# Kernel tuning notes

Measured on AMD Instinct MI355X. Metric: run time of the kernel, lower is better.

The kernel has to match this reference:

```python
import jax, jax.numpy as jnp
import numpy as np

NSIDE = 128
NPIX = 12 * NSIDE * NSIDE          # HEALPix pixel count, nested ordering
WIN = 16                           # window = 4x4 nested child block (w=1)
SHIFT = WIN // 2
EPS = 1e-5


def _ln(x, g, b):
    mu = x.mean(-1, keepdims=True)
    var = ((x - mu) ** 2).mean(-1, keepdims=True)
    return (x - mu) * jax.lax.rsqrt(var + EPS) * g + b


def _window_attn(x, wq, bq, wp, bp, n_heads):
    B, N, C = x.shape
    D = C // n_heads
    nw = N // WIN
    qkv = (x @ wq + bq).reshape(B, nw, WIN, 3, n_heads, D)
    q, k, v = jnp.moveaxis(qkv, 3, 0)
    q = jnp.swapaxes(q, 2, 3)
    k = jnp.swapaxes(k, 2, 3)
    v = jnp.swapaxes(v, 2, 3)
    scores = jnp.einsum('bwhqd,bwhkd->bwhqk', q, k) * (D ** -0.5)
    attn = jax.nn.softmax(scores, axis=-1)
    out = jnp.einsum('bwhqk,bwhkd->bwhqd', attn, v)
    out = jnp.swapaxes(out, 2, 3).reshape(B, N, C)
    return out @ wp + bp


def _transformer_block(x, p, shift, n_heads):
    if shift:
        x = jnp.roll(x, -SHIFT, axis=1)          # cyclic shift along nested index
    x = x + _window_attn(_ln(x, p['ln1_g'], p['ln1_b']),
                         p['w_qkv'], p['b_qkv'], p['w_proj'], p['b_proj'], n_heads)
    h = _ln(x, p['ln2_g'], p['ln2_b'])
    x = x + jax.nn.gelu(h @ p['w_mlp1'] + p['b_mlp1'], approximate=False) @ p['w_mlp2'] + p['b_mlp2']
    if shift:
        x = jnp.roll(x, SHIFT, axis=1)
    return x


def _forward(x, w_ff1, b_ff1, ln1_g, ln1_b, w_qkv, b_qkv, w_proj, b_proj,
             ln2_g, ln2_b, w_mlp1, b_mlp1, w_mlp2, b_mlp2, w_ff2, b_ff2,
             n_heads=4):
    residual = x
    h = jax.nn.gelu(x @ w_ff1 + b_ff1, approximate=False)
    for i, shift in enumerate((False, True)):
        p = dict(ln1_g=ln1_g[i], ln1_b=ln1_b[i], w_qkv=w_qkv[i], b_qkv=b_qkv[i],
                 w_proj=w_proj[i], b_proj=b_proj[i], ln2_g=ln2_g[i], ln2_b=ln2_b[i],
                 w_mlp1=w_mlp1[i], b_mlp1=b_mlp1[i], w_mlp2=w_mlp2[i], b_mlp2=b_mlp2[i])
        h = _transformer_block(h, p, shift, n_heads)
    return residual + h @ w_ff2 + b_ff2


def setup_inputs() -> dict:
    key = jax.random.key(0)
    ks = jax.random.split(key, 8)
    F, C, M = 64, 128, 512  # node_feat_dim, node_hidden_dim, mlp hidden
    s = 0.02
    return {
        'x': jax.random.normal(ks[0], (1, NPIX, F), jnp.float32),
        'w_ff1': jax.random.normal(ks[1], (F, C), jnp.float32) * s,
        'b_ff1': jnp.zeros((C,), jnp.float32),
        'ln1_g': jnp.ones((2, C), jnp.float32),
        'ln1_b': jnp.zeros((2, C), jnp.float32),
        'w_qkv': jax.random.normal(ks[2], (2, C, 3 * C), jnp.float32) * s,
        'b_qkv': jnp.zeros((2, 3 * C), jnp.float32),
        'w_proj': jax.random.normal(ks[3], (2, C, C), jnp.float32) * s,
        'b_proj': jnp.zeros((2, C), jnp.float32),
        'ln2_g': jnp.ones((2, C), jnp.float32),
        'ln2_b': jnp.zeros((2, C), jnp.float32),
        'w_mlp1': jax.random.normal(ks[4], (2, C, M), jnp.float32) * s,
        'b_mlp1': jnp.zeros((2, M), jnp.float32),
        'w_mlp2': jax.random.normal(ks[5], (2, M, C), jnp.float32) * s,
        'b_mlp2': jnp.zeros((2, C), jnp.float32),
        'w_ff2': jax.random.normal(ks[6], (C, F), jnp.float32) * s,
        'b_ff2': jnp.zeros((F,), jnp.float32),
    }


def reference(x, w_ff1, b_ff1, ln1_g, ln1_b, w_qkv, b_qkv, w_proj, b_proj,
              ln2_g, ln2_b, w_mlp1, b_mlp1, w_mlp2, b_mlp2, w_ff2, b_ff2):
    return _forward(x, w_ff1, b_ff1, ln1_g, ln1_b, w_qkv, b_qkv, w_proj, b_proj,
                    ln2_g, ln2_b, w_mlp1, b_mlp1, w_mlp2, b_mlp2, w_ff2, b_ff2)
```

## Files before the change

### kernel.cpp

```cpp
#include <hip/hip_runtime.h>
#include <hip/hip_bf16.h>
#include <math.h>

#define NPIX 196608
#define SCALE_Q 0.17677669529663687f

typedef __attribute__((ext_vector_type(4))) float f32x4;
typedef __attribute__((ext_vector_type(8))) short short8;
typedef __attribute__((ext_vector_type(4))) short short4v;
typedef __hip_bfloat16 bf16;

__device__ __forceinline__ float gelu_f(float x) {
    float yy = 1.5957691216057308f * (x + 0.044715f * x * x * x);
    float e = __expf(yy);
    return x - x * __builtin_amdgcn_rcpf(e + 1.0f);
}
__device__ __forceinline__ float gelu_fast(float x) {
    float e = __expf(-1.702f * x);
    return x * __builtin_amdgcn_rcpf(1.0f + e);
}

__device__ __forceinline__ short bfbits(float f) {
    bf16 h = __float2bfloat16(f);
    return *reinterpret_cast<short*>(&h);
}

__device__ __forceinline__ short8 ldsA(const bf16* buf, int row, int el) {
    return *reinterpret_cast<const short8*>(buf + row * 128 + (el ^ ((row & 7) << 3)));
}
__device__ __forceinline__ short8 ldsA64(const bf16* buf, int row, int el) {
    return *reinterpret_cast<const short8*>(buf + row * 64 + (el ^ ((row & 7) << 3)));
}
__device__ __forceinline__ short8 gld8(const bf16* p) {
    return *reinterpret_cast<const short8*>(p);
}

__device__ __forceinline__ void bar_lds() {
    asm volatile("s_waitcnt lgkmcnt(0)" ::: "memory");
    __builtin_amdgcn_s_barrier();
}

__global__ __launch_bounds__(256) void k_convert(
    const float* __restrict__ wff1, const float* __restrict__ wqkv,
    const float* __restrict__ wproj, const float* __restrict__ wmlp1,
    const float* __restrict__ wmlp2, const float* __restrict__ wff2,
    bf16* __restrict__ dst)
{
    int gid = blockIdx.x * 256 + threadIdx.x;
    if (gid < 8192) {
        int n = gid >> 6, k = gid & 63;
        dst[gid] = __float2bfloat16(wff1[k * 128 + n]);
    } else if (gid < 106496) {
        int r = gid - 8192; int l = r / 49152; r -= l * 49152;
        int n = r >> 7, k = r & 127;
        dst[gid] = __float2bfloat16(wqkv[l * 49152 + k * 384 + n]);
    } else if (gid < 139264) {
        int r = gid - 106496; int l = r / 16384; r -= l * 16384;
        int n = r >> 7, k = r & 127;
        dst[gid] = __float2bfloat16(wproj[l * 16384 + k * 128 + n]);
    } else if (gid < 270336) {
        int r = gid - 139264; int l = r >> 16; r &= 65535;
        int n = r >> 7, k = r & 127;
        dst[gid] = __float2bfloat16(wmlp1[l * 65536 + k * 512 + n]);
    } else if (gid < 401408) {
        int r = gid - 270336; int l = r >> 16; r &= 65535;
        int n = r >> 9, k = r & 511;
        dst[gid] = __float2bfloat16(wmlp2[l * 65536 + k * 128 + n]);
    } else if (gid < 409600) {
        int r = gid - 401408;
        int n = r >> 7, k = r & 127;
        dst[gid] = __float2bfloat16(wff2[k * 64 + n]);
    }
}

template <int OFFSET, int MODE>
__global__ __launch_bounds__(256, 3) void k_block(
    const float* __restrict__ x, float* __restrict__ h,
    const bf16* __restrict__ wf1t, const float* __restrict__ bf1,
    const float* __restrict__ g1, const float* __restrict__ be1,
    const bf16* __restrict__ wqt, const float* __restrict__ bq,
    const bf16* __restrict__ wpt, const float* __restrict__ bp,
    const float* __restrict__ g2, const float* __restrict__ be2,
    const bf16* __restrict__ w1t, const float* __restrict__ b1,
    const bf16* __restrict__ w2t, const float* __restrict__ b2,
    const bf16* __restrict__ wf2t, const float* __restrict__ bf2,
    float* __restrict__ out)
{
    __shared__ bf16 bufA[8192];
    __shared__ bf16 bufB[8192];
    __shared__ bf16 bufC[8192];
    const int tid = threadIdx.x, base = blockIdx.x * 64;
    const int wid = tid >> 6, lrow = tid & 15, lgrp = (tid >> 4) & 3;
    const int cb0 = wid * 32;
    const int hc  = wid * 32;

    f32x4 hraw[2][4];

    if (MODE == 0) {
        short8 wf1[2][2];
#pragma unroll
        for (int nt = 0; nt < 2; ++nt)
#pragma unroll
            for (int kk = 0; kk < 2; ++kk)
                wf1[nt][kk] = gld8(wf1t + (size_t)(cb0 + nt * 16 + lrow) * 64 + kk * 32 + lgrp * 8);
        {
            int row = tid >> 2, q = tid & 3;
#pragma unroll
            for (int s = 0; s < 2; ++s) {
                int gg = q + s * 4;
                const float4* src = reinterpret_cast<const float4*>(x + (size_t)(base + row) * 64 + gg * 8);
                float4 v0 = src[0], v1 = src[1];
                short8 w;
                w[0] = bfbits(v0.x); w[1] = bfbits(v0.y); w[2] = bfbits(v0.z); w[3] = bfbits(v0.w);
                w[4] = bfbits(v1.x); w[5] = bfbits(v1.y); w[6] = bfbits(v1.z); w[7] = bfbits(v1.w);
                *reinterpret_cast<short8*>(&bufC[row * 64 + ((gg * 8) ^ ((row & 7) << 3))]) = w;
            }
        }
        bar_lds();
        short8 xb1[4][2];
#pragma unroll
        for (int tt = 0; tt < 4; ++tt)
#pragma unroll
            for (int kk = 0; kk < 2; ++kk)
                xb1[tt][kk] = ldsA64(bufC, tt * 16 + lrow, kk * 32 + lgrp * 8);
        bar_lds();
#pragma unroll
        for (int nt = 0; nt < 2; ++nt) {
            float4 bv = *reinterpret_cast<const float4*>(bf1 + cb0 + nt * 16 + lgrp * 4);
#pragma unroll
            for (int tt = 0; tt < 4; ++tt) {
                f32x4 d = {0.f, 0.f, 0.f, 0.f};
#pragma unroll
                for (int kk = 0; kk < 2; ++kk)
                    d = __builtin_amdgcn_mfma_f32_16x16x32_bf16(wf1[nt][kk], xb1[tt][kk], d, 0, 0, 0);
                f32x4 r;
                r[0] = gelu_f(d[0] + bv.x); r[1] = gelu_f(d[1] + bv.y);
                r[2] = gelu_f(d[2] + bv.z); r[3] = gelu_f(d[3] + bv.w);
                hraw[nt][tt] = r;
            }
        }
    } else {
#pragma unroll
        for (int nt = 0; nt < 2; ++nt)
#pragma unroll
            for (int tt = 0; tt < 4; ++tt) {
                int tok = base + OFFSET + tt * 16 + lrow; if (tok >= NPIX) tok -= NPIX;
                float4 hv = *reinterpret_cast<const float4*>(h + (size_t)tok * 128 + cb0 + nt * 16 + lgrp * 4);
                f32x4 r; r[0] = hv.x; r[1] = hv.y; r[2] = hv.z; r[3] = hv.w;
                hraw[nt][tt] = r;
            }
    }

    float2* ws = reinterpret_cast<float2*>(bufC);
#pragma unroll
    for (int tt = 0; tt < 4; ++tt) {
        float s = 0.f, q = 0.f;
#pragma unroll
        for (int nt = 0; nt < 2; ++nt)
#pragma unroll
            for (int i = 0; i < 4; ++i) { float v = hraw[nt][tt][i]; s += v; q += v * v; }
        s += __shfl_xor(s, 16, 64); s += __shfl_xor(s, 32, 64);
        q += __shfl_xor(q, 16, 64); q += __shfl_xor(q, 32, 64);
        if (lgrp == 0) { float2 t2; t2.x = s; t2.y = q; ws[wid * 64 + tt * 16 + lrow] = t2; }
    }
    bar_lds();
    {
        float mu[4], rstd[4];
#pragma unroll
        for (int tt = 0; tt < 4; ++tt) {
            float s = 0.f, q = 0.f;
#pragma unroll
            for (int w = 0; w < 4; ++w) {
                float2 t2 = ws[w * 64 + tt * 16 + lrow];
                s += t2.x; q += t2.y;
            }
            float m = s * (1.f / 128.f);
            mu[tt] = m;
            rstd[tt] = rsqrtf(q * (1.f / 128.f) - m * m + 1e-5f);
        }
        float4 gv[2], bev[2];
#pragma unroll
        for (int nt = 0; nt < 2; ++nt) {
            gv[nt]  = *reinterpret_cast<const float4*>(g1 + cb0 + nt * 16 + lgrp * 4);
            bev[nt] = *reinterpret_cast<const float4*>(be1 + cb0 + nt * 16 + lgrp * 4);
        }
#pragma unroll
        for (int nt = 0; nt < 2; ++nt)
#pragma unroll
            for (int tt = 0; tt < 4; ++tt) {
                short4v pk;
                pk[0] = bfbits((hraw[nt][tt][0] - mu[tt]) * rstd[tt] * gv[nt].x + bev[nt].x);
                pk[1] = bfbits((hraw[nt][tt][1] - mu[tt]) * rstd[tt] * gv[nt].y + bev[nt].y);
                pk[2] = bfbits((hraw[nt][tt][2] - mu[tt]) * rstd[tt] * gv[nt].z + bev[nt].z);
                pk[3] = bfbits((hraw[nt][tt][3] - mu[tt]) * rstd[tt] * gv[nt].w + bev[nt].w);
                int row = tt * 16 + lrow;
                int c = cb0 + nt * 16 + lgrp * 4;
                *reinterpret_cast<short4v*>(&bufA[row * 128 + (c ^ ((row & 7) << 3))]) = pk;
            }
    }
    short8 wfp[2][4];
#pragma unroll
    for (int nt = 0; nt < 2; ++nt)
#pragma unroll
        for (int kk = 0; kk < 4; ++kk)
            wfp[nt][kk] = gld8(wpt + (size_t)(cb0 + nt * 16 + lrow) * 128 + kk * 32 + lgrp * 8);
    bar_lds();

    short8 xb[4][4];
#pragma unroll
    for (int tt = 0; tt < 4; ++tt)
#pragma unroll
        for (int kk = 0; kk < 4; ++kk)
            xb[tt][kk] = ldsA(bufA, tt * 16 + lrow, kk * 32 + lgrp * 8);
    bar_lds();

#pragma unroll
    for (int qt = 0; qt < 2; ++qt) {
        const int cb = hc + qt * 16;
        float4 bqv = *reinterpret_cast<const float4*>(bq + cb + lgrp * 4);
        short8 wf[4];
#pragma unroll
        for (int kk = 0; kk < 4; ++kk)
            wf[kk] = gld8(wqt + (size_t)(cb + lrow) * 128 + kk * 32 + lgrp * 8);
#pragma unroll
        for (int tt = 0; tt < 4; ++tt) {
            f32x4 d = {0.f, 0.f, 0.f, 0.f};
#pragma unroll
            for (int kk = 0; kk < 4; ++kk)
                d = __builtin_amdgcn_mfma_f32_16x16x32_bf16(wf[kk], xb[tt][kk], d, 0, 0, 0);
            int row = tt * 16 + lrow;
            int c = cb + lgrp * 4;
            short4v pk;
            pk[0] = bfbits((d[0] + bqv.x) * SCALE_Q); pk[1] = bfbits((d[1] + bqv.y) * SCALE_Q);
            pk[2] = bfbits((d[2] + bqv.z) * SCALE_Q); pk[3] = bfbits((d[3] + bqv.w) * SCALE_Q);
            *reinterpret_cast<short4v*>(&bufA[row * 128 + (c ^ ((row & 7) << 3))]) = pk;
        }
    }
#pragma unroll
    for (int kt = 0; kt < 2; ++kt) {
        const int cb = hc + kt * 16;
        float4 bqv = *reinterpret_cast<const float4*>(bq + 128 + cb + lgrp * 4);
        short8 wf[4];
#pragma unroll
        for (int kk = 0; kk < 4; ++kk)
            wf[kk] = gld8(wqt + (size_t)(128 + cb + lrow) * 128 + kk * 32 + lgrp * 8);
#pragma unroll
        for (int tt = 0; tt < 4; ++tt) {
            f32x4 d = {0.f, 0.f, 0.f, 0.f};
#pragma unroll
            for (int kk = 0; kk < 4; ++kk)
                d = __builtin_amdgcn_mfma_f32_16x16x32_bf16(wf[kk], xb[tt][kk], d, 0, 0, 0);
            int row = tt * 16 + lrow;
            int c = cb + lgrp * 4;
            short4v pk;
            pk[0] = bfbits(d[0] + bqv.x); pk[1] = bfbits(d[1] + bqv.y);
            pk[2] = bfbits(d[2] + bqv.z); pk[3] = bfbits(d[3] + bqv.w);
            *reinterpret_cast<short4v*>(&bufB[row * 128 + (c ^ ((row & 7) << 3))]) = pk;
        }
    }
    bf16* vt = bufC + wid * 2048;
#pragma unroll
    for (int vt_ = 0; vt_ < 2; ++vt_) {
        const int cb = hc + vt_ * 16;
        float4 bqv = *reinterpret_cast<const float4*>(bq + 256 + cb + lgrp * 4);
        short8 wf[4];
#pragma unroll
        for (int kk = 0; kk < 4; ++kk)
            wf[kk] = gld8(wqt + (size_t)(256 + cb + lrow) * 128 + kk * 32 + lgrp * 8);
#pragma unroll
        for (int tt = 0; tt < 4; ++tt) {
            f32x4 d = {0.f, 0.f, 0.f, 0.f};
#pragma unroll
            for (int kk = 0; kk < 4; ++kk)
                d = __builtin_amdgcn_mfma_f32_16x16x32_bf16(wf[kk], xb[tt][kk], d, 0, 0, 0);
#pragma unroll
            for (int i = 0; i < 4; ++i)
                vt[(vt_ * 16 + lgrp * 4 + i) * 64 + tt * 16 + lrow] =
                    __float2bfloat16(d[i] + ((const float*)&bqv)[i]);
        }
    }

#pragma unroll
    for (int tt = 0; tt < 4; ++tt) {
        const int row = tt * 16 + lrow;
        const int swr = (lrow & 7) << 3;
        short8 aq = *reinterpret_cast<const short8*>(&bufA[row * 128 + ((hc + lgrp * 8) ^ swr)]);
        short8 bk = *reinterpret_cast<const short8*>(&bufB[row * 128 + ((hc + lgrp * 8) ^ swr)]);
        f32x4 z = {0.f, 0.f, 0.f, 0.f};
        f32x4 s = __builtin_amdgcn_mfma_f32_16x16x32_bf16(bk, aq, z, 0, 0, 0);
        float m_ = fmaxf(fmaxf(s[0], s[1]), fmaxf(s[2], s[3]));
        m_ = fmaxf(m_, __shfl_xor(m_, 16, 64));
        m_ = fmaxf(m_, __shfl_xor(m_, 32, 64));
        float e0 = __expf(s[0] - m_), e1 = __expf(s[1] - m_);
        float e2 = __expf(s[2] - m_), e3 = __expf(s[3] - m_);
        float sum = e0 + e1 + e2 + e3;
        sum += __shfl_xor(sum, 16, 64);
        sum += __shfl_xor(sum, 32, 64);
        float r = __builtin_amdgcn_rcpf(sum);
        short4v pp;
        pp[0] = bfbits(e0 * r); pp[1] = bfbits(e1 * r);
        pp[2] = bfbits(e2 * r); pp[3] = bfbits(e3 * r);
        *reinterpret_cast<short4v*>(&bufA[row * 128 + ((hc + lgrp * 4) ^ swr)]) = pp;

        short8 z8 = {0, 0, 0, 0, 0, 0, 0, 0};
        short8 bp_ = z8;
        if (lgrp < 2)
            bp_ = *reinterpret_cast<const short8*>(&bufA[row * 128 + ((hc + lgrp * 8) ^ swr)]);
#pragma unroll
        for (int dt = 0; dt < 2; ++dt) {
            short8 av = z8;
            if (lgrp < 2)
                av = *reinterpret_cast<const short8*>(&vt[(dt * 16 + lrow) * 64 + tt * 16 + lgrp * 8]);
            f32x4 o = __builtin_amdgcn_mfma_f32_16x16x32_bf16(av, bp_, z, 0, 0, 0);
            short4v pk;
            pk[0] = bfbits(o[0]); pk[1] = bfbits(o[1]); pk[2] = bfbits(o[2]); pk[3] = bfbits(o[3]);
            *reinterpret_cast<short4v*>(&bufA[row * 128 + ((hc + dt * 16 + lgrp * 4) ^ swr)]) = pk;
        }
    }
    bar_lds();

    short8 af[4][4];
#pragma unroll
    for (int tt = 0; tt < 4; ++tt)
#pragma unroll
        for (int kk = 0; kk < 4; ++kk)
            af[tt][kk] = ldsA(bufA, tt * 16 + lrow, kk * 32 + lgrp * 8);
    f32x4 hres[2][4];
#pragma unroll
    for (int nt = 0; nt < 2; ++nt) {
        float4 bpv = *reinterpret_cast<const float4*>(bp + cb0 + nt * 16 + lgrp * 4);
#pragma unroll
        for (int tt = 0; tt < 4; ++tt) {
            f32x4 d = {0.f, 0.f, 0.f, 0.f};
#pragma unroll
            for (int kk = 0; kk < 4; ++kk)
                d = __builtin_amdgcn_mfma_f32_16x16x32_bf16(wfp[nt][kk], af[tt][kk], d, 0, 0, 0);
            f32x4 r = hraw[nt][tt];
            r[0] += bpv.x + d[0]; r[1] += bpv.y + d[1];
            r[2] += bpv.z + d[2]; r[3] += bpv.w + d[3];
            hres[nt][tt] = r;
        }
    }

#pragma unroll
    for (int tt = 0; tt < 4; ++tt) {
        float s = 0.f, q = 0.f;
#pragma unroll
        for (int nt = 0; nt < 2; ++nt)
#pragma unroll
            for (int i = 0; i < 4; ++i) { float v = hres[nt][tt][i]; s += v; q += v * v; }
        s += __shfl_xor(s, 16, 64); s += __shfl_xor(s, 32, 64);
        q += __shfl_xor(q, 16, 64); q += __shfl_xor(q, 32, 64);
        if (lgrp == 0) { float2 t2; t2.x = s; t2.y = q; ws[wid * 64 + tt * 16 + lrow] = t2; }
    }
    bar_lds();
    short8 w1f[2][2][4];
    {
        float mu[4], rstd[4];
#pragma unroll
        for (int tt = 0; tt < 4; ++tt) {
            float s = 0.f, q = 0.f;
#pragma unroll
            for (int w = 0; w < 4; ++w) {
                float2 t2 = ws[w * 64 + tt * 16 + lrow];
                s += t2.x; q += t2.y;
            }
            float m = s * (1.f / 128.f);
            mu[tt] = m;
            rstd[tt] = rsqrtf(q * (1.f / 128.f) - m * m + 1e-5f);
        }
        float4 gv[2], bev[2];
#pragma unroll
        for (int nt = 0; nt < 2; ++nt) {
            gv[nt]  = *reinterpret_cast<const float4*>(g2 + cb0 + nt * 16 + lgrp * 4);
            bev[nt] = *reinterpret_cast<const float4*>(be2 + cb0 + nt * 16 + lgrp * 4);
        }
#pragma unroll
        for (int nt = 0; nt < 2; ++nt)
#pragma unroll
            for (int tt = 0; tt < 4; ++tt) {
                short4v pk;
                pk[0] = bfbits((hres[nt][tt][0] - mu[tt]) * rstd[tt] * gv[nt].x + bev[nt].x);
                pk[1] = bfbits((hres[nt][tt][1] - mu[tt]) * rstd[tt] * gv[nt].y + bev[nt].y);
                pk[2] = bfbits((hres[nt][tt][2] - mu[tt]) * rstd[tt] * gv[nt].z + bev[nt].z);
                pk[3] = bfbits((hres[nt][tt][3] - mu[tt]) * rstd[tt] * gv[nt].w + bev[nt].w);
                int row = tt * 16 + lrow;
                int c = cb0 + nt * 16 + lgrp * 4;
                *reinterpret_cast<short4v*>(&bufB[row * 128 + (c ^ ((row & 7) << 3))]) = pk;
            }
    }
#pragma unroll
    for (int nt = 0; nt < 2; ++nt)
#pragma unroll
        for (int kk = 0; kk < 4; ++kk)
            w1f[0][nt][kk] = gld8(w1t + (size_t)(cb0 + nt * 16 + lrow) * 128 + kk * 32 + lgrp * 8);
    bar_lds();

    f32x4 acc2[2][4];
#pragma unroll
    for (int nt = 0; nt < 2; ++nt)
#pragma unroll
        for (int tt = 0; tt < 4; ++tt) acc2[nt][tt] = (f32x4){0.f, 0.f, 0.f, 0.f};

#pragma unroll
    for (int ch = 0; ch < 4; ++ch) {
        bf16* UB = (ch & 1) ? bufC : bufA;
        short8 w2f[2][4];
#pragma unroll
        for (int nt = 0; nt < 2; ++nt)
#pragma unroll
            for (int kk = 0; kk < 4; ++kk)
                w2f[nt][kk] = gld8(w2t + (size_t)(cb0 + nt * 16 + lrow) * 512 + ch * 128 + kk * 32 + lgrp * 8);
        float4 b1v[2];
#pragma unroll
        for (int nt = 0; nt < 2; ++nt)
            b1v[nt] = *reinterpret_cast<const float4*>(b1 + ch * 128 + cb0 + nt * 16 + lgrp * 4);
#pragma unroll
        for (int tt = 0; tt < 4; ++tt) {
            short8 xf[4];
#pragma unroll
            for (int kk = 0; kk < 4; ++kk)
                xf[kk] = ldsA(bufB, tt * 16 + lrow, kk * 32 + lgrp * 8);
#pragma unroll
            for (int nt = 0; nt < 2; ++nt) {
                f32x4 d = {0.f, 0.f, 0.f, 0.f};
#pragma unroll
                for (int kk = 0; kk < 4; ++kk)
                    d = __builtin_amdgcn_mfma_f32_16x16x32_bf16(w1f[ch & 1][nt][kk], xf[kk], d, 0, 0, 0);
                short4v pk;
                pk[0] = bfbits(gelu_fast(d[0] + b1v[nt].x)); pk[1] = bfbits(gelu_fast(d[1] + b1v[nt].y));
                pk[2] = bfbits(gelu_fast(d[2] + b1v[nt].z)); pk[3] = bfbits(gelu_fast(d[3] + b1v[nt].w));
                int row = tt * 16 + lrow;
                int c = cb0 + nt * 16 + lgrp * 4;
                *reinterpret_cast<short4v*>(&UB[row * 128 + (c ^ ((row & 7) << 3))]) = pk;
            }
        }
        if (ch < 3) {
#pragma unroll
            for (int nt = 0; nt < 2; ++nt)
#pragma unroll
                for (int kk = 0; kk < 4; ++kk)
                    w1f[(ch + 1) & 1][nt][kk] =
                        gld8(w1t + (size_t)((ch + 1) * 128 + cb0 + nt * 16 + lrow) * 128 + kk * 32 + lgrp * 8);
        }
        bar_lds();
#pragma unroll
        for (int tt = 0; tt < 4; ++tt) {
            short8 uf[4];
#pragma unroll
            for (int kk = 0; kk < 4; ++kk)
                uf[kk] = ldsA(UB, tt * 16 + lrow, kk * 32 + lgrp * 8);
#pragma unroll
            for (int nt = 0; nt < 2; ++nt)
#pragma unroll
                for (int kk = 0; kk < 4; ++kk)
                    acc2[nt][tt] = __builtin_amdgcn_mfma_f32_16x16x32_bf16(
                        w2f[nt][kk], uf[kk], acc2[nt][tt], 0, 0, 0);
        }
    }

    if (MODE == 0) {
#pragma unroll
        for (int nt = 0; nt < 2; ++nt) {
            const int n0 = cb0 + nt * 16 + lgrp * 4;
            float4 b2v = *reinterpret_cast<const float4*>(b2 + n0);
#pragma unroll
            for (int tt = 0; tt < 4; ++tt) {
                int tok = base + OFFSET + tt * 16 + lrow; if (tok >= NPIX) tok -= NPIX;
                float4 ov;
                ov.x = hres[nt][tt][0] + b2v.x + acc2[nt][tt][0];
                ov.y = hres[nt][tt][1] + b2v.y + acc2[nt][tt][1];
                ov.z = hres[nt][tt][2] + b2v.z + acc2[nt][tt][2];
                ov.w = hres[nt][tt][3] + b2v.w + acc2[nt][tt][3];
                *reinterpret_cast<float4*>(h + (size_t)tok * 128 + n0) = ov;
            }
        }
    } else {
        short8 wff[4];
#pragma unroll
        for (int kk = 0; kk < 4; ++kk)
            wff[kk] = gld8(wf2t + (size_t)(wid * 16 + lrow) * 128 + kk * 32 + lgrp * 8);
        float4 xv[4];
#pragma unroll
        for (int tt = 0; tt < 4; ++tt) {
            int tok = base + OFFSET + tt * 16 + lrow; if (tok >= NPIX) tok -= NPIX;
            xv[tt] = *reinterpret_cast<const float4*>(x + (size_t)tok * 64 + wid * 16 + lgrp * 4);
        }
        bar_lds();
#pragma unroll
        for (int nt = 0; nt < 2; ++nt) {
            const int n0 = cb0 + nt * 16 + lgrp * 4;
            float4 b2v = *reinterpret_cast<const float4*>(b2 + n0);
#pragma unroll
            for (int tt = 0; tt < 4; ++tt) {
                short4v pk;
                pk[0] = bfbits(hres[nt][tt][0] + b2v.x + acc2[nt][tt][0]);
                pk[1] = bfbits(hres[nt][tt][1] + b2v.y + acc2[nt][tt][1]);
                pk[2] = bfbits(hres[nt][tt][2] + b2v.z + acc2[nt][tt][2]);
                pk[3] = bfbits(hres[nt][tt][3] + b2v.w + acc2[nt][tt][3]);
                int row = tt * 16 + lrow;
                int c = cb0 + nt * 16 + lgrp * 4;
                *reinterpret_cast<short4v*>(&bufB[row * 128 + (c ^ ((row & 7) << 3))]) = pk;
            }
        }
        bar_lds();
        float4 bfv = *reinterpret_cast<const float4*>(bf2 + wid * 16 + lgrp * 4);
#pragma unroll
        for (int tt = 0; tt < 4; ++tt) {
            short8 bfr[4];
#pragma unroll
            for (int kk = 0; kk < 4; ++kk)
                bfr[kk] = ldsA(bufB, tt * 16 + lrow, kk * 32 + lgrp * 8);
            f32x4 d = {0.f, 0.f, 0.f, 0.f};
#pragma unroll
            for (int kk = 0; kk < 4; ++kk)
                d = __builtin_amdgcn_mfma_f32_16x16x32_bf16(wff[kk], bfr[kk], d, 0, 0, 0);
            int tok = base + OFFSET + tt * 16 + lrow; if (tok >= NPIX) tok -= NPIX;
            float4 ov;
            ov.x = xv[tt].x + bfv.x + d[0]; ov.y = xv[tt].y + bfv.y + d[1];
            ov.z = xv[tt].z + bfv.z + d[2]; ov.w = xv[tt].w + bfv.w + d[3];
            *reinterpret_cast<float4*>(out + (size_t)tok * 64 + wid * 16 + lgrp * 4) = ov;
        }
    }
}

extern "C" void kernel_launch(void* const* d_in, const int* in_sizes, int n_in,
                              void* d_out, int out_size, void* d_ws, size_t ws_size,
                              hipStream_t stream) {
    (void)in_sizes; (void)n_in; (void)out_size; (void)ws_size;
    const float* x      = (const float*)d_in[0];
    const float* w_ff1  = (const float*)d_in[1];
    const float* b_ff1  = (const float*)d_in[2];
    const float* ln1_g  = (const float*)d_in[3];
    const float* ln1_b  = (const float*)d_in[4];
    const float* w_qkv  = (const float*)d_in[5];
    const float* b_qkv  = (const float*)d_in[6];
    const float* w_proj = (const float*)d_in[7];
    const float* b_proj = (const float*)d_in[8];
    const float* ln2_g  = (const float*)d_in[9];
    const float* ln2_b  = (const float*)d_in[10];
    const float* w_mlp1 = (const float*)d_in[11];
    const float* b_mlp1 = (const float*)d_in[12];
    const float* w_mlp2 = (const float*)d_in[13];
    const float* b_mlp2 = (const float*)d_in[14];
    const float* w_ff2  = (const float*)d_in[15];
    const float* b_ff2  = (const float*)d_in[16];
    float* out = (float*)d_out;

    float* h = (float*)d_ws;
    bf16* wbf = (bf16*)((char*)d_ws + (size_t)NPIX * 128 * 4);
    bf16* ff1t  = wbf;
    bf16* qkvt  = wbf + 8192;
    bf16* projt = wbf + 106496;
    bf16* mlp1t = wbf + 139264;
    bf16* mlp2t = wbf + 270336;
    bf16* ff2t  = wbf + 401408;

    k_convert<<<1600, dim3(256), 0, stream>>>(w_ff1, w_qkv, w_proj, w_mlp1, w_mlp2, w_ff2, wbf);

    const int NB = NPIX / 64;
    k_block<0, 0><<<NB, dim3(256), 0, stream>>>(x, h,
        ff1t, b_ff1,
        ln1_g, ln1_b, qkvt, b_qkv, projt, b_proj,
        ln2_g, ln2_b, mlp1t, b_mlp1, mlp2t, b_mlp2,
        ff2t, b_ff2, out);

    k_block<8, 1><<<NB, dim3(256), 0, stream>>>(x, h,
        ff1t, b_ff1,
        ln1_g + 128, ln1_b + 128, qkvt + 49152, b_qkv + 384, projt + 16384, b_proj + 128,
        ln2_g + 128, ln2_b + 128, mlp1t + 65536, b_mlp1 + 512, mlp2t + 65536, b_mlp2 + 128,
        ff2t, b_ff2, out);
}
```

Measured before the change: 407.9 us.

## Fold LayerNorm mean/rstd and beta into GEMM epilogues via precomputed weight sums

A small kernel precomputes, per output column, the gamma-weighted and beta-weighted column sums of the QKV and MLP1 weights, with the bias folded in. The main kernel then feeds only x*gamma into the MFMA and applies rstd*d - rstd*mu*c1 + c2 in the epilogue. This takes the LayerNorm statistics reduction off the path before the GEMM operand is written, removing one barrier wait ahead of each GEMM. The cost is an extra launch, more epilogue arithmetic, and possible bf16 precision loss because un-normalized activations are quantized before the matmul and the mean is subtracted afterward.

```diff
diff --git a/kernel.cpp b/kernel.cpp
--- a/kernel.cpp
+++ b/kernel.cpp
@@ -73,17 +73,53 @@
     }
 }
 
+__global__ __launch_bounds__(256) void k_fold(
+    const float* __restrict__ wqkv, const float* __restrict__ wmlp1,
+    const float* __restrict__ g1, const float* __restrict__ be1,
+    const float* __restrict__ bqv,
+    const float* __restrict__ g2, const float* __restrict__ be2,
+    const float* __restrict__ b1,
+    float* __restrict__ c1q, float* __restrict__ c2q,
+    float* __restrict__ c1m, float* __restrict__ c2m)
+{
+    int gid = blockIdx.x * 256 + threadIdx.x;
+    if (gid < 768) {
+        int l = gid / 384, j = gid - l * 384;
+        float a = 0.f, b = 0.f;
+        for (int k = 0; k < 128; ++k) {
+            float w = __bfloat162float(__float2bfloat16(wqkv[l * 49152 + k * 384 + j]));
+            a += g1[l * 128 + k] * w;
+            b += be1[l * 128 + k] * w;
+        }
+        c1q[gid] = a;
+        c2q[gid] = b + bqv[l * 384 + j];
+    } else if (gid < 1792) {
+        int r = gid - 768;
+        int l = r >> 9, j = r & 511;
+        float a = 0.f, b = 0.f;
+        for (int k = 0; k < 128; ++k) {
+            float w = __bfloat162float(__float2bfloat16(wmlp1[l * 65536 + k * 512 + j]));
+            a += g2[l * 128 + k] * w;
+            b += be2[l * 128 + k] * w;
+        }
+        c1m[r] = a;
+        c2m[r] = b + b1[l * 512 + j];
+    }
+}
+
 template <int OFFSET, int MODE>
 __global__ __launch_bounds__(256, 3) void k_block(
     const float* __restrict__ x, float* __restrict__ h,
     const bf16* __restrict__ wf1t, const float* __restrict__ bf1,
-    const float* __restrict__ g1, const float* __restrict__ be1,
-    const bf16* __restrict__ wqt, const float* __restrict__ bq,
+    const float* __restrict__ g1,
+    const bf16* __restrict__ wqt,
     const bf16* __restrict__ wpt, const float* __restrict__ bp,
-    const float* __restrict__ g2, const float* __restrict__ be2,
-    const bf16* __restrict__ w1t, const float* __restrict__ b1,
+    const float* __restrict__ g2,
+    const bf16* __restrict__ w1t,
     const bf16* __restrict__ w2t, const float* __restrict__ b2,
     const bf16* __restrict__ wf2t, const float* __restrict__ bf2,
+    const float* __restrict__ c1q, const float* __restrict__ c2q,
+    const float* __restrict__ c1m, const float* __restrict__ c2m,
     float* __restrict__ out)
 {
     __shared__ bf16 bufA[8192];
@@ -163,36 +199,20 @@
         q += __shfl_xor(q, 16, 64); q += __shfl_xor(q, 32, 64);
         if (lgrp == 0) { float2 t2; t2.x = s; t2.y = q; ws[wid * 64 + tt * 16 + lrow] = t2; }
     }
-    bar_lds();
     {
-        float mu[4], rstd[4];
-#pragma unroll
-        for (int tt = 0; tt < 4; ++tt) {
-            float s = 0.f, q = 0.f;
-#pragma unroll
-            for (int w = 0; w < 4; ++w) {
-                float2 t2 = ws[w * 64 + tt * 16 + lrow];
-                s += t2.x; q += t2.y;
-            }
-            float m = s * (1.f / 128.f);
-            mu[tt] = m;
-            rstd[tt] = rsqrtf(q * (1.f / 128.f) - m * m + 1e-5f);
-        }
-        float4 gv[2], bev[2];
-#pragma unroll
-        for (int nt = 0; nt < 2; ++nt) {
-            gv[nt]  = *reinterpret_cast<const float4*>(g1 + cb0 + nt * 16 + lgrp * 4);
-            bev[nt] = *reinterpret_cast<const float4*>(be1 + cb0 + nt * 16 + lgrp * 4);
-        }
+        float4 gv[2];
+#pragma unroll
+        for (int nt = 0; nt < 2; ++nt)
+            gv[nt] = *reinterpret_cast<const float4*>(g1 + cb0 + nt * 16 + lgrp * 4);
 #pragma unroll
         for (int nt = 0; nt < 2; ++nt)
 #pragma unroll
             for (int tt = 0; tt < 4; ++tt) {
                 short4v pk;
-                pk[0] = bfbits((hraw[nt][tt][0] - mu[tt]) * rstd[tt] * gv[nt].x + bev[nt].x);
-                pk[1] = bfbits((hraw[nt][tt][1] - mu[tt]) * rstd[tt] * gv[nt].y + bev[nt].y);
-                pk[2] = bfbits((hraw[nt][tt][2] - mu[tt]) * rstd[tt] * gv[nt].z + bev[nt].z);
-                pk[3] = bfbits((hraw[nt][tt][3] - mu[tt]) * rstd[tt] * gv[nt].w + bev[nt].w);
+                pk[0] = bfbits(hraw[nt][tt][0] * gv[nt].x);
+                pk[1] = bfbits(hraw[nt][tt][1] * gv[nt].y);
+                pk[2] = bfbits(hraw[nt][tt][2] * gv[nt].z);
+                pk[3] = bfbits(hraw[nt][tt][3] * gv[nt].w);
                 int row = tt * 16 + lrow;
                 int c = cb0 + nt * 16 + lgrp * 4;
                 *reinterpret_cast<short4v*>(&bufA[row * 128 + (c ^ ((row & 7) << 3))]) = pk;
@@ -206,6 +226,19 @@
             wfp[nt][kk] = gld8(wpt + (size_t)(cb0 + nt * 16 + lrow) * 128 + kk * 32 + lgrp * 8);
     bar_lds();
 
+    float rstd1[4], rmu1[4];
+#pragma unroll
+    for (int tt = 0; tt < 4; ++tt) {
+        float s = 0.f, q = 0.f;
+#pragma unroll
+        for (int w = 0; w < 4; ++w) {
+            float2 t2 = ws[w * 64 + tt * 16 + lrow];
+            s += t2.x; q += t2.y;
+        }
+        float m = s * (1.f / 128.f);
+        float rs = rsqrtf(q * (1.f / 128.f) - m * m + 1e-5f);
+        rstd1[tt] = rs; rmu1[tt] = rs * m;
+    }
     short8 xb[4][4];
 #pragma unroll
     for (int tt = 0; tt < 4; ++tt)
@@ -217,7 +250,8 @@
 #pragma unroll
     for (int qt = 0; qt < 2; ++qt) {
         const int cb = hc + qt * 16;
-        float4 bqv = *reinterpret_cast<const float4*>(bq + cb + lgrp * 4);
+        float4 c1v = *reinterpret_cast<const float4*>(c1q + cb + lgrp * 4);
+        float4 c2v = *reinterpret_cast<const float4*>(c2q + cb + lgrp * 4);
         short8 wf[4];
 #pragma unroll
         for (int kk = 0; kk < 4; ++kk)
@@ -230,16 +264,20 @@
                 d = __builtin_amdgcn_mfma_f32_16x16x32_bf16(wf[kk], xb[tt][kk], d, 0, 0, 0);
             int row = tt * 16 + lrow;
             int c = cb + lgrp * 4;
+            float rs = rstd1[tt], rm = rmu1[tt];
             short4v pk;
-            pk[0] = bfbits((d[0] + bqv.x) * SCALE_Q); pk[1] = bfbits((d[1] + bqv.y) * SCALE_Q);
-            pk[2] = bfbits((d[2] + bqv.z) * SCALE_Q); pk[3] = bfbits((d[3] + bqv.w) * SCALE_Q);
+            pk[0] = bfbits((rs * d[0] - rm * c1v.x + c2v.x) * SCALE_Q);
+            pk[1] = bfbits((rs * d[1] - rm * c1v.y + c2v.y) * SCALE_Q);
+            pk[2] = bfbits((rs * d[2] - rm * c1v.z + c2v.z) * SCALE_Q);
+            pk[3] = bfbits((rs * d[3] - rm * c1v.w + c2v.w) * SCALE_Q);
             *reinterpret_cast<short4v*>(&bufA[row * 128 + (c ^ ((row & 7) << 3))]) = pk;
         }
     }
 #pragma unroll
     for (int kt = 0; kt < 2; ++kt) {
         const int cb = hc + kt * 16;
-        float4 bqv = *reinterpret_cast<const float4*>(bq + 128 + cb + lgrp * 4);
+        float4 c1v = *reinterpret_cast<const float4*>(c1q + 128 + cb + lgrp * 4);
+        float4 c2v = *reinterpret_cast<const float4*>(c2q + 128 + cb + lgrp * 4);
         short8 wf[4];
 #pragma unroll
         for (int kk = 0; kk < 4; ++kk)
@@ -252,9 +290,12 @@
                 d = __builtin_amdgcn_mfma_f32_16x16x32_bf16(wf[kk], xb[tt][kk], d, 0, 0, 0);
             int row = tt * 16 + lrow;
             int c = cb + lgrp * 4;
+            float rs = rstd1[tt], rm = rmu1[tt];
             short4v pk;
-            pk[0] = bfbits(d[0] + bqv.x); pk[1] = bfbits(d[1] + bqv.y);
-            pk[2] = bfbits(d[2] + bqv.z); pk[3] = bfbits(d[3] + bqv.w);
+            pk[0] = bfbits(rs * d[0] - rm * c1v.x + c2v.x);
+            pk[1] = bfbits(rs * d[1] - rm * c1v.y + c2v.y);
+            pk[2] = bfbits(rs * d[2] - rm * c1v.z + c2v.z);
+            pk[3] = bfbits(rs * d[3] - rm * c1v.w + c2v.w);
             *reinterpret_cast<short4v*>(&bufB[row * 128 + (c ^ ((row & 7) << 3))]) = pk;
         }
     }
@@ -262,7 +303,8 @@
 #pragma unroll
     for (int vt_ = 0; vt_ < 2; ++vt_) {
         const int cb = hc + vt_ * 16;
-        float4 bqv = *reinterpret_cast<const float4*>(bq + 256 + cb + lgrp * 4);
+        float4 c1v = *reinterpret_cast<const float4*>(c1q + 256 + cb + lgrp * 4);
+        float4 c2v = *reinterpret_cast<const float4*>(c2q + 256 + cb + lgrp * 4);
         short8 wf[4];
 #pragma unroll
         for (int kk = 0; kk < 4; ++kk)
@@ -273,10 +315,11 @@
 #pragma unroll
             for (int kk = 0; kk < 4; ++kk)
                 d = __builtin_amdgcn_mfma_f32_16x16x32_bf16(wf[kk], xb[tt][kk], d, 0, 0, 0);
-#pragma unroll
-            for (int i = 0; i < 4; ++i)
-                vt[(vt_ * 16 + lgrp * 4 + i) * 64 + tt * 16 + lrow] =
-                    __float2bfloat16(d[i] + ((const float*)&bqv)[i]);
+            float rs = rstd1[tt], rm = rmu1[tt];
+            vt[(vt_ * 16 + lgrp * 4 + 0) * 64 + tt * 16 + lrow] = __float2bfloat16(rs * d[0] - rm * c1v.x + c2v.x);
+            vt[(vt_ * 16 + lgrp * 4 + 1) * 64 + tt * 16 + lrow] = __float2bfloat16(rs * d[1] - rm * c1v.y + c2v.y);
+            vt[(vt_ * 16 + lgrp * 4 + 2) * 64 + tt * 16 + lrow] = __float2bfloat16(rs * d[2] - rm * c1v.z + c2v.z);
+            vt[(vt_ * 16 + lgrp * 4 + 3) * 64 + tt * 16 + lrow] = __float2bfloat16(rs * d[3] - rm * c1v.w + c2v.w);
         }
     }
 
@@ -353,48 +396,46 @@
         q += __shfl_xor(q, 16, 64); q += __shfl_xor(q, 32, 64);
         if (lgrp == 0) { float2 t2; t2.x = s; t2.y = q; ws[wid * 64 + tt * 16 + lrow] = t2; }
     }
-    bar_lds();
-    short8 w1f[2][2][4];
     {
-        float mu[4], rstd[4];
-#pragma unroll
-        for (int tt = 0; tt < 4; ++tt) {
-            float s = 0.f, q = 0.f;
-#pragma unroll
-            for (int w = 0; w < 4; ++w) {
-                float2 t2 = ws[w * 64 + tt * 16 + lrow];
-                s += t2.x; q += t2.y;
-            }
-            float m = s * (1.f / 128.f);
-            mu[tt] = m;
-            rstd[tt] = rsqrtf(q * (1.f / 128.f) - m * m + 1e-5f);
-        }
-        float4 gv[2], bev[2];
-#pragma unroll
-        for (int nt = 0; nt < 2; ++nt) {
-            gv[nt]  = *reinterpret_cast<const float4*>(g2 + cb0 + nt * 16 + lgrp * 4);
-            bev[nt] = *reinterpret_cast<const float4*>(be2 + cb0 + nt * 16 + lgrp * 4);
-        }
+        float4 gv2[2];
+#pragma unroll
+        for (int nt = 0; nt < 2; ++nt)
+            gv2[nt] = *reinterpret_cast<const float4*>(g2 + cb0 + nt * 16 + lgrp * 4);
 #pragma unroll
         for (int nt = 0; nt < 2; ++nt)
 #pragma unroll
             for (int tt = 0; tt < 4; ++tt) {
                 short4v pk;
-                pk[0] = bfbits((hres[nt][tt][0] - mu[tt]) * rstd[tt] * gv[nt].x + bev[nt].x);
-                pk[1] = bfbits((hres[nt][tt][1] - mu[tt]) * rstd[tt] * gv[nt].y + bev[nt].y);
-                pk[2] = bfbits((hres[nt][tt][2] - mu[tt]) * rstd[tt] * gv[nt].z + bev[nt].z);
-                pk[3] = bfbits((hres[nt][tt][3] - mu[tt]) * rstd[tt] * gv[nt].w + bev[nt].w);
+                pk[0] = bfbits(hres[nt][tt][0] * gv2[nt].x);
+                pk[1] = bfbits(hres[nt][tt][1] * gv2[nt].y);
+                pk[2] = bfbits(hres[nt][tt][2] * gv2[nt].z);
+                pk[3] = bfbits(hres[nt][tt][3] * gv2[nt].w);
                 int row = tt * 16 + lrow;
                 int c = cb0 + nt * 16 + lgrp * 4;
                 *reinterpret_cast<short4v*>(&bufB[row * 128 + (c ^ ((row & 7) << 3))]) = pk;
             }
     }
+    short8 w1f[2][2][4];
 #pragma unroll
     for (int nt = 0; nt < 2; ++nt)
 #pragma unroll
         for (int kk = 0; kk < 4; ++kk)
             w1f[0][nt][kk] = gld8(w1t + (size_t)(cb0 + nt * 16 + lrow) * 128 + kk * 32 + lgrp * 8);
     bar_lds();
+
+    float rstd2[4], rmu2[4];
+#pragma unroll
+    for (int tt = 0; tt < 4; ++tt) {
+        float s = 0.f, q = 0.f;
+#pragma unroll
+        for (int w = 0; w < 4; ++w) {
+            float2 t2 = ws[w * 64 + tt * 16 + lrow];
+            s += t2.x; q += t2.y;
+        }
+        float m = s * (1.f / 128.f);
+        float rs = rsqrtf(q * (1.f / 128.f) - m * m + 1e-5f);
+        rstd2[tt] = rs; rmu2[tt] = rs * m;
+    }
 
     f32x4 acc2[2][4];
 #pragma unroll
@@ -411,10 +452,12 @@
 #pragma unroll
             for (int kk = 0; kk < 4; ++kk)
                 w2f[nt][kk] = gld8(w2t + (size_t)(cb0 + nt * 16 + lrow) * 512 + ch * 128 + kk * 32 + lgrp * 8);
-        float4 b1v[2];
-#pragma unroll
-        for (int nt = 0; nt < 2; ++nt)
-            b1v[nt] = *reinterpret_cast<const float4*>(b1 + ch * 128 + cb0 + nt * 16 + lgrp * 4);
+        float4 c1mv[2], c2mv[2];
+#pragma unroll
+        for (int nt = 0; nt < 2; ++nt) {
+            c1mv[nt] = *reinterpret_cast<const float4*>(c1m + ch * 128 + cb0 + nt * 16 + lgrp * 4);
+            c2mv[nt] = *reinterpret_cast<const float4*>(c2m + ch * 128 + cb0 + nt * 16 + lgrp * 4);
+        }
 #pragma unroll
         for (int tt = 0; tt < 4; ++tt) {
             short8 xf[4];
@@ -427,9 +470,12 @@
 #pragma unroll
                 for (int kk = 0; kk < 4; ++kk)
                     d = __builtin_amdgcn_mfma_f32_16x16x32_bf16(w1f[ch & 1][nt][kk], xf[kk], d, 0, 0, 0);
+                float rs = rstd2[tt], rm = rmu2[tt];
                 short4v pk;
-                pk[0] = bfbits(gelu_fast(d[0] + b1v[nt].x)); pk[1] = bfbits(gelu_fast(d[1] + b1v[nt].y));
-                pk[2] = bfbits(gelu_fast(d[2] + b1v[nt].z)); pk[3] = bfbits(gelu_fast(d[3] + b1v[nt].w));
+                pk[0] = bfbits(gelu_fast(rs * d[0] - rm * c1mv[nt].x + c2mv[nt].x));
+                pk[1] = bfbits(gelu_fast(rs * d[1] - rm * c1mv[nt].y + c2mv[nt].y));
+                pk[2] = bfbits(gelu_fast(rs * d[2] - rm * c1mv[nt].z + c2mv[nt].z));
+                pk[3] = bfbits(gelu_fast(rs * d[3] - rm * c1mv[nt].w + c2mv[nt].w));
                 int row = tt * 16 + lrow;
                 int c = cb0 + nt * 16 + lgrp * 4;
                 *reinterpret_cast<short4v*>(&UB[row * 128 + (c ^ ((row & 7) << 3))]) = pk;
@@ -555,19 +601,28 @@
     bf16* mlp1t = wbf + 139264;
     bf16* mlp2t = wbf + 270336;
     bf16* ff2t  = wbf + 401408;
+    float* cf   = (float*)((char*)wbf + 819200);
+    float* c1q  = cf;
+    float* c2q  = cf + 768;
+    float* c1m  = cf + 1536;
+    float* c2m  = cf + 2560;
 
     k_convert<<<1600, dim3(256), 0, stream>>>(w_ff1, w_qkv, w_proj, w_mlp1, w_mlp2, w_ff2, wbf);
+    k_fold<<<7, dim3(256), 0, stream>>>(w_qkv, w_mlp1, ln1_g, ln1_b, b_qkv,
+                                        ln2_g, ln2_b, b_mlp1, c1q, c2q, c1m, c2m);
 
     const int NB = NPIX / 64;
     k_block<0, 0><<<NB, dim3(256), 0, stream>>>(x, h,
         ff1t, b_ff1,
-        ln1_g, ln1_b, qkvt, b_qkv, projt, b_proj,
-        ln2_g, ln2_b, mlp1t, b_mlp1, mlp2t, b_mlp2,
-        ff2t, b_ff2, out);
+        ln1_g, qkvt, projt, b_proj,
+        ln2_g, mlp1t, mlp2t, b_mlp2,
+        ff2t, b_ff2,
+        c1q, c2q, c1m, c2m, out);
 
     k_block<8, 1><<<NB, dim3(256), 0, stream>>>(x, h,
         ff1t, b_ff1,
-        ln1_g + 128, ln1_b + 128, qkvt + 49152, b_qkv + 384, projt + 16384, b_proj + 128,
-        ln2_g + 128, ln2_b + 128, mlp1t + 65536, b_mlp1 + 512, mlp2t + 65536, b_mlp2 + 128,
-        ff2t, b_ff2, out);
-}
+        ln1_g + 128, qkvt + 49152, projt + 16384, b_proj + 128,
+        ln2_g + 128, mlp1t + 65536, mlp2t + 65536, b_mlp2 + 128,
+        ff2t, b_ff2,
+        c1q + 384, c2q + 384, c1m + 512, c2m + 512, out);
+}
```

Result: slower. 459.3 us (+12.6%).
